# Performance work log

Measured on AMD Instinct MI355X. Metric: run time of the kernel, lower is better.

Reference implementation:

```python
import jax, jax.numpy as jnp
import numpy as np

SCALE = 1.0 / np.sqrt(128.0)  # 1/sqrt(head_size)
NEG = -1000000000.0


def setup_inputs() -> dict:
    key = jax.random.key(0)
    k1, k2, k3, k4 = jax.random.split(key, 4)
    B, H, S, D = 2, 16, 2048, 128
    q = jax.random.normal(k1, (B, H, S, D), dtype=jnp.float32)
    k = jax.random.normal(k2, (B, H, S, D), dtype=jnp.float32)
    v = jax.random.normal(k3, (B, H, S, D), dtype=jnp.float32)
    mask = jax.random.randint(k4, (B, S), 0, 2, dtype=jnp.int32)
    return {"q": q, "k": k, "v": v, "mask": mask}


def reference(q, k, v, mask):
    # scores: [B, H, Sq, Sk]
    scores = jnp.einsum("bhqd,bhkd->bhqk", q, k) * SCALE
    m = mask[:, None, None, :]  # [B,1,1,Sk], broadcast over heads and queries
    scores = jnp.where(m == 0, NEG, scores)
    weights = jax.nn.softmax(scores, axis=-1)
    out = jnp.einsum("bhqk,bhkd->bhqd", weights, v)
    return out
```

## Files before the change

### kernel.cpp

```cpp
#include <hip/hip_runtime.h>
#include <hip/hip_bf16.h>

typedef __attribute__((ext_vector_type(8))) short short8;
typedef __attribute__((ext_vector_type(4))) short short4v;
typedef __attribute__((ext_vector_type(4))) float floatx4;

#define NB 2
#define NH 16
#define NBH 32
#define SS 2048
#define DD 128
#define BQ 128
#define BK 32
#define KTILES (SS / BK)
#define SCALE 0.08838834764831845f
#define LOG2E 1.4426950408889634f
#define MAXB 12.0f
#define MASKED_BIAS -100000.0f

#define WC_VM4 0x0F74
#define WC_VM0 0x0F70
#define WC_LGKM0 0xC07F

__device__ __forceinline__ short f2bf(float f) {
  union { float f; unsigned u; } x; x.f = f;
  return (short)((x.u + 0x7FFFu + ((x.u >> 16) & 1u)) >> 16);
}

__device__ __forceinline__ void pack8(short8* dst, float a, float b, float c, float d,
                                      float e, float f, float g, float h) {
  union { __hip_bfloat162 h2[4]; short8 v; } u;
  u.h2[0] = __float22bfloat162_rn(make_float2(a, b));
  u.h2[1] = __float22bfloat162_rn(make_float2(c, d));
  u.h2[2] = __float22bfloat162_rn(make_float2(e, f));
  u.h2[3] = __float22bfloat162_rn(make_float2(g, h));
  *dst = u.v;
}

__device__ __forceinline__ void gload_lds16(const short* g, short* l) {
  __builtin_amdgcn_global_load_lds(
      (const __attribute__((address_space(1))) void*)(g),
      (__attribute__((address_space(3))) void*)(l), 16, 0, 0);
}

__global__ __launch_bounds__(256) void prep_kernel(const float* __restrict__ k,
                                                   const float* __restrict__ v,
                                                   short* __restrict__ kbf,
                                                   short* __restrict__ vtg) {
  __shared__ short Ts[DD][68];
  const int kb = blockIdx.x, bh = blockIdx.y;
  const int tid = threadIdx.x;
  const size_t base = (size_t)bh * SS * DD + (size_t)(kb * 64) * DD;
  const float* kr = k + base;
  const float* vr = v + base;
  short* kw = kbf + base;
#pragma unroll
  for (int c = 0; c < 8; ++c) {
    int fi = c * 256 + tid;
    float4 a = ((const float4*)kr)[fi];
    short4v o;
    o[0] = f2bf(a.x); o[1] = f2bf(a.y); o[2] = f2bf(a.z); o[3] = f2bf(a.w);
    *(short4v*)(kw + (size_t)fi * 4) = o;
    float4 vv = ((const float4*)vr)[fi];
    int d0 = (fi * 4) & 127, key = (fi * 4) >> 7;
    Ts[d0 + 0][key] = f2bf(vv.x);
    Ts[d0 + 1][key] = f2bf(vv.y);
    Ts[d0 + 2][key] = f2bf(vv.z);
    Ts[d0 + 3][key] = f2bf(vv.w);
  }
  __syncthreads();
#pragma unroll
  for (int s = 0; s < 4; ++s) {
    int d = s * 32 + (tid >> 3);
    int c = tid & 7, kt2 = c >> 2, g = c & 3;
    short4v lo = *(short4v*)&Ts[d][kt2 * 32 + g * 4];
    short4v hi = *(short4v*)&Ts[d][kt2 * 32 + 16 + g * 4];
    short8 o;
#pragma unroll
    for (int r = 0; r < 4; ++r) { o[r] = lo[r]; o[4 + r] = hi[r]; }
    *(short8*)(vtg + ((size_t)(bh * DD + d)) * SS + (kb * 2 + kt2) * 32 + g * 8) = o;
  }
}

__global__ __launch_bounds__(256, 2) void fa_kernel(
    const float* __restrict__ q, const short* __restrict__ kbf,
    const short* __restrict__ vtg, const int* __restrict__ mask,
    float* __restrict__ out) {
  __shared__ __align__(16) short Ks[3][BK * DD];
  __shared__ __align__(16) short Vt[3][DD * BK];
  __shared__ float Bias[SS];

  const int tid = threadIdx.x;
  const int wave = tid >> 6;
  const int lane = tid & 63;
  const int l16 = lane & 15;
  const int quad = lane >> 4;
  const int bh = blockIdx.y;
  const int b = bh >> 4;
  const int q0 = blockIdx.x * BQ;

  const size_t base = (size_t)bh * SS * DD;
  const float* qg = q + base;
  const short* kg = kbf + base;
  const short* vgb = vtg + (size_t)bh * DD * SS;
  const int* mg = mask + b * SS;
  const float c1 = SCALE * LOG2E, c2 = MAXB * LOG2E;

  short8 qf[2][4];
#pragma unroll
  for (int t = 0; t < 2; ++t) {
    const float* qp = qg + (size_t)(q0 + wave * 32 + t * 16 + l16) * DD;
#pragma unroll
    for (int dc = 0; dc < 4; ++dc) {
      float4 a = *(const float4*)(qp + dc * 32 + quad * 8);
      float4 bb = *(const float4*)(qp + dc * 32 + quad * 8 + 4);
      short8 tt;
      tt[0] = f2bf(a.x); tt[1] = f2bf(a.y); tt[2] = f2bf(a.z); tt[3] = f2bf(a.w);
      tt[4] = f2bf(bb.x); tt[5] = f2bf(bb.y); tt[6] = f2bf(bb.z); tt[7] = f2bf(bb.w);
      qf[t][dc] = tt;
    }
  }

  {
    int i0 = tid * 8;
    int4 m0 = *(const int4*)(mg + i0);
    int4 m1 = *(const int4*)(mg + i0 + 4);
    float4 f0, f1;
    f0.x = m0.x ? -c2 : MASKED_BIAS; f0.y = m0.y ? -c2 : MASKED_BIAS;
    f0.z = m0.z ? -c2 : MASKED_BIAS; f0.w = m0.w ? -c2 : MASKED_BIAS;
    f1.x = m1.x ? -c2 : MASKED_BIAS; f1.y = m1.y ? -c2 : MASKED_BIAS;
    f1.z = m1.z ? -c2 : MASKED_BIAS; f1.w = m1.w ? -c2 : MASKED_BIAS;
    *(float4*)&Bias[i0] = f0;
    *(float4*)&Bias[i0 + 4] = f1;
  }

  floatx4 Oacc[2][8];
#pragma unroll
  for (int t = 0; t < 2; ++t)
#pragma unroll
    for (int f = 0; f < 8; ++f) Oacc[t][f] = (floatx4){0.f, 0.f, 0.f, 0.f};
  float l_acc[2] = {0.f, 0.f};

  const short* kpg[2];
  const short* vpg[2];
  int kls[2], vls[2];
#pragma unroll
  for (int i = 0; i < 2; ++i) {
    int c = wave * 2 + i;
    int krow = c * 4 + (lane >> 4);
    kpg[i] = kg + (size_t)krow * DD + (((lane & 15) ^ (krow & 7)) * 8);
    int d = c * 16 + (lane >> 2);
    vpg[i] = vgb + (size_t)d * SS + (((lane & 3) ^ ((lane >> 3) & 3)) * 8);
    kls[i] = c * 512;
    vls[i] = c * 512;
  }

  int koff[2];
#pragma unroll
  for (int nt = 0; nt < 2; ++nt) koff[nt] = (nt * 16 + l16) * DD;
  const int ksw = l16 & 7;
  const int voff = l16 * 32 + ((quad ^ ((l16 >> 1) & 3)) * 8);

#pragma unroll
  for (int i = 0; i < 2; ++i) {
    gload_lds16(kpg[i], &Ks[0][kls[i]]);
    gload_lds16(vpg[i], &Vt[0][vls[i]]);
  }
#pragma unroll
  for (int i = 0; i < 2; ++i) {
    gload_lds16(kpg[i] + (size_t)BK * DD, &Ks[1][kls[i]]);
    gload_lds16(vpg[i] + BK, &Vt[1][vls[i]]);
  }
  __builtin_amdgcn_s_waitcnt(WC_LGKM0);

  int cur = 0;
#pragma unroll 1
  for (int kt = 0; kt < KTILES; ++kt) {
    if (kt + 1 < KTILES) __builtin_amdgcn_s_waitcnt(WC_VM4);
    else                 __builtin_amdgcn_s_waitcnt(WC_VM0);
    __builtin_amdgcn_s_barrier();

    int ibuf = cur + 2; if (ibuf >= 3) ibuf -= 3;
    if (kt + 2 < KTILES) {
      const size_t kadv = (size_t)(kt + 2) * (BK * DD);
      const int vadv = (kt + 2) * BK;
#pragma unroll
      for (int i = 0; i < 2; ++i) {
        gload_lds16(kpg[i] + kadv, &Ks[ibuf][kls[i]]);
        gload_lds16(vpg[i] + vadv, &Vt[ibuf][vls[i]]);
      }
    }

    float4 bb0 = *(const float4*)&Bias[kt * 32 + quad * 4];
    float4 bb1 = *(const float4*)&Bias[kt * 32 + 16 + quad * 4];

    const short* ksb = &Ks[cur][0];
    const short* vsb = &Vt[cur][0];
    floatx4 sacc[2][2];
#pragma unroll
    for (int t = 0; t < 2; ++t)
#pragma unroll
      for (int nt = 0; nt < 2; ++nt) sacc[t][nt] = (floatx4){0.f, 0.f, 0.f, 0.f};
#pragma unroll
    for (int nt = 0; nt < 2; ++nt)
#pragma unroll
      for (int dc = 0; dc < 4; ++dc) {
        short8 kf = *(const short8*)(ksb + koff[nt] + (((dc * 4 + quad) ^ ksw) * 8));
        sacc[0][nt] = __builtin_amdgcn_mfma_f32_16x16x32_bf16(kf, qf[0][dc], sacc[0][nt], 0, 0, 0);
        sacc[1][nt] = __builtin_amdgcn_mfma_f32_16x16x32_bf16(kf, qf[1][dc], sacc[1][nt], 0, 0, 0);
      }

    short8 pb[2];
#pragma unroll
    for (int t = 0; t < 2; ++t) {
      float e0 = __builtin_amdgcn_exp2f(fmaf(sacc[t][0][0], c1, bb0.x));
      float e1 = __builtin_amdgcn_exp2f(fmaf(sacc[t][0][1], c1, bb0.y));
      float e2 = __builtin_amdgcn_exp2f(fmaf(sacc[t][0][2], c1, bb0.z));
      float e3 = __builtin_amdgcn_exp2f(fmaf(sacc[t][0][3], c1, bb0.w));
      float g0 = __builtin_amdgcn_exp2f(fmaf(sacc[t][1][0], c1, bb1.x));
      float g1 = __builtin_amdgcn_exp2f(fmaf(sacc[t][1][1], c1, bb1.y));
      float g2 = __builtin_amdgcn_exp2f(fmaf(sacc[t][1][2], c1, bb1.z));
      float g3 = __builtin_amdgcn_exp2f(fmaf(sacc[t][1][3], c1, bb1.w));
      l_acc[t] += ((e0 + e1) + (e2 + e3)) + ((g0 + g1) + (g2 + g3));
      pack8(&pb[t], e0, e1, e2, e3, g0, g1, g2, g3);
    }

#pragma unroll
    for (int f = 0; f < 8; ++f) {
      short8 vv = *(const short8*)(vsb + f * 512 + voff);
      Oacc[0][f] = __builtin_amdgcn_mfma_f32_16x16x32_bf16(vv, pb[0], Oacc[0][f], 0, 0, 0);
      Oacc[1][f] = __builtin_amdgcn_mfma_f32_16x16x32_bf16(vv, pb[1], Oacc[1][f], 0, 0, 0);
    }

    cur = cur + 1; if (cur >= 3) cur = 0;
  }

  float* og = out + base;
#pragma unroll
  for (int t = 0; t < 2; ++t) {
    float s = l_acc[t];
    s += __shfl_xor(s, 16);
    s += __shfl_xor(s, 32);
    float inv = 1.0f / s;
    float* orow = og + (size_t)(q0 + wave * 32 + t * 16 + l16) * DD + quad * 4;
#pragma unroll
    for (int f = 0; f < 8; ++f) {
      float4 w;
      w.x = Oacc[t][f][0] * inv;
      w.y = Oacc[t][f][1] * inv;
      w.z = Oacc[t][f][2] * inv;
      w.w = Oacc[t][f][3] * inv;
      *(float4*)(orow + f * 16) = w;
    }
  }
}

extern "C" void kernel_launch(void* const* d_in, const int* in_sizes, int n_in,
                              void* d_out, int out_size, void* d_ws, size_t ws_size,
                              hipStream_t stream) {
  const float* q = (const float*)d_in[0];
  const float* k = (const float*)d_in[1];
  const float* v = (const float*)d_in[2];
  const int* mask = (const int*)d_in[3];
  float* out = (float*)d_out;

  short* kbf = (short*)d_ws;
  short* vtg = kbf + (size_t)NBH * SS * DD;

  prep_kernel<<<dim3(SS / 64, NBH), dim3(256), 0, stream>>>(k, v, kbf, vtg);
  fa_kernel<<<dim3(SS / BQ, NBH), dim3(256), 0, stream>>>(q, kbf, vtg, mask, out);
}
```

Baseline: 210.7 us.

## Swizzle prep transpose, remap blocks, stagger K start, move prefetch after QK, set priorities

The prep kernel's V transpose now loads 4x4 float4 blocks and writes XOR-swizzled short4 vectors into LDS, replacing scalar padded stores, to cut LDS bank conflicts. The attention kernel remaps block IDs so neighbouring blocks spread across heads, and some heads start the K-tile loop at an offset, aiming to reduce L2/HBM hotspotting on the same K/V tiles. The next-tile prefetch is issued after the QK MFMAs instead of before, and s_setprio raises wave priority around the MFMA sections to interleave math with other waves' softmax. These changes bundle several unrelated ideas and could shift scheduling in either direction.

```diff
diff --git a/kernel.cpp b/kernel.cpp
--- a/kernel.cpp
+++ b/kernel.cpp
@@ -47,13 +47,14 @@
                                                    const float* __restrict__ v,
                                                    short* __restrict__ kbf,
                                                    short* __restrict__ vtg) {
-  __shared__ short Ts[DD][68];
+  __shared__ __align__(16) short Ts[DD * 64];
   const int kb = blockIdx.x, bh = blockIdx.y;
   const int tid = threadIdx.x;
   const size_t base = (size_t)bh * SS * DD + (size_t)(kb * 64) * DD;
   const float* kr = k + base;
   const float* vr = v + base;
   short* kw = kbf + base;
+
 #pragma unroll
   for (int c = 0; c < 8; ++c) {
     int fi = c * 256 + tid;
@@ -61,20 +62,38 @@
     short4v o;
     o[0] = f2bf(a.x); o[1] = f2bf(a.y); o[2] = f2bf(a.z); o[3] = f2bf(a.w);
     *(short4v*)(kw + (size_t)fi * 4) = o;
-    float4 vv = ((const float4*)vr)[fi];
-    int d0 = (fi * 4) & 127, key = (fi * 4) >> 7;
-    Ts[d0 + 0][key] = f2bf(vv.x);
-    Ts[d0 + 1][key] = f2bf(vv.y);
-    Ts[d0 + 2][key] = f2bf(vv.z);
-    Ts[d0 + 3][key] = f2bf(vv.w);
+  }
+
+  const int kg = tid & 15;
+  const int dg0 = tid >> 4;
+#pragma unroll
+  for (int c = 0; c < 2; ++c) {
+    int dg = dg0 + 16 * c;
+    float rr[4][4];
+#pragma unroll
+    for (int r = 0; r < 4; ++r) {
+      float4 a = ((const float4*)vr)[(kg * 4 + r) * 32 + dg];
+      rr[r][0] = a.x; rr[r][1] = a.y; rr[r][2] = a.z; rr[r][3] = a.w;
+    }
+#pragma unroll
+    for (int j = 0; j < 4; ++j) {
+      int d = dg * 4 + j;
+      short4v t;
+      t[0] = f2bf(rr[0][j]); t[1] = f2bf(rr[1][j]);
+      t[2] = f2bf(rr[2][j]); t[3] = f2bf(rr[3][j]);
+      int si = d * 64 + (((kg * 8) ^ ((d & 15) << 3)) >> 1);
+      *(short4v*)&Ts[si] = t;
+    }
   }
   __syncthreads();
+
 #pragma unroll
   for (int s = 0; s < 4; ++s) {
     int d = s * 32 + (tid >> 3);
     int c = tid & 7, kt2 = c >> 2, g = c & 3;
-    short4v lo = *(short4v*)&Ts[d][kt2 * 32 + g * 4];
-    short4v hi = *(short4v*)&Ts[d][kt2 * 32 + 16 + g * 4];
+    int x = (d & 15) << 3;
+    short4v lo = *(short4v*)&Ts[d * 64 + ((((kt2 * 8 + g) * 8) ^ x) >> 1)];
+    short4v hi = *(short4v*)&Ts[d * 64 + ((((kt2 * 8 + g + 4) * 8) ^ x) >> 1)];
     short8 o;
 #pragma unroll
     for (int r = 0; r < 4; ++r) { o[r] = lo[r]; o[4 + r] = hi[r]; }
@@ -95,9 +114,13 @@
   const int lane = tid & 63;
   const int l16 = lane & 15;
   const int quad = lane >> 4;
-  const int bh = blockIdx.y;
+
+  const int lid = blockIdx.y * 16 + blockIdx.x;
+  const int vid = (lid & 7) * 64 + (lid >> 3);
+  const int bh = vid >> 4;
+  const int q0 = (vid & 15) * BQ;
   const int b = bh >> 4;
-  const int q0 = blockIdx.x * BQ;
+  const int kt0off = ((bh >> 1) & 1) << 5;
 
   const size_t base = (size_t)bh * SS * DD;
   const float* qg = q + base;
@@ -161,35 +184,29 @@
   const int ksw = l16 & 7;
   const int voff = l16 * 32 + ((quad ^ ((l16 >> 1) & 3)) * 8);
 
-#pragma unroll
-  for (int i = 0; i < 2; ++i) {
-    gload_lds16(kpg[i], &Ks[0][kls[i]]);
-    gload_lds16(vpg[i], &Vt[0][vls[i]]);
-  }
-#pragma unroll
-  for (int i = 0; i < 2; ++i) {
-    gload_lds16(kpg[i] + (size_t)BK * DD, &Ks[1][kls[i]]);
-    gload_lds16(vpg[i] + BK, &Vt[1][vls[i]]);
+  {
+    const size_t ka0 = (size_t)kt0off * (BK * DD);
+    const int va0 = kt0off * BK;
+#pragma unroll
+    for (int i = 0; i < 2; ++i) {
+      gload_lds16(kpg[i] + ka0, &Ks[0][kls[i]]);
+      gload_lds16(vpg[i] + va0, &Vt[0][vls[i]]);
+    }
+#pragma unroll
+    for (int i = 0; i < 2; ++i) {
+      gload_lds16(kpg[i] + ka0 + (size_t)(BK * DD), &Ks[1][kls[i]]);
+      gload_lds16(vpg[i] + va0 + BK, &Vt[1][vls[i]]);
+    }
   }
   __builtin_amdgcn_s_waitcnt(WC_LGKM0);
 
   int cur = 0;
 #pragma unroll 1
-  for (int kt = 0; kt < KTILES; ++kt) {
-    if (kt + 1 < KTILES) __builtin_amdgcn_s_waitcnt(WC_VM4);
+  for (int it = 0; it < KTILES; ++it) {
+    const int kt = (it + kt0off) & (KTILES - 1);
+    if (it + 1 < KTILES) __builtin_amdgcn_s_waitcnt(WC_VM4);
     else                 __builtin_amdgcn_s_waitcnt(WC_VM0);
     __builtin_amdgcn_s_barrier();
-
-    int ibuf = cur + 2; if (ibuf >= 3) ibuf -= 3;
-    if (kt + 2 < KTILES) {
-      const size_t kadv = (size_t)(kt + 2) * (BK * DD);
-      const int vadv = (kt + 2) * BK;
-#pragma unroll
-      for (int i = 0; i < 2; ++i) {
-        gload_lds16(kpg[i] + kadv, &Ks[ibuf][kls[i]]);
-        gload_lds16(vpg[i] + vadv, &Vt[ibuf][vls[i]]);
-      }
-    }
 
     float4 bb0 = *(const float4*)&Bias[kt * 32 + quad * 4];
     float4 bb1 = *(const float4*)&Bias[kt * 32 + 16 + quad * 4];
@@ -201,6 +218,7 @@
     for (int t = 0; t < 2; ++t)
 #pragma unroll
       for (int nt = 0; nt < 2; ++nt) sacc[t][nt] = (floatx4){0.f, 0.f, 0.f, 0.f};
+    __builtin_amdgcn_s_setprio(1);
 #pragma unroll
     for (int nt = 0; nt < 2; ++nt)
 #pragma unroll
@@ -209,6 +227,19 @@
         sacc[0][nt] = __builtin_amdgcn_mfma_f32_16x16x32_bf16(kf, qf[0][dc], sacc[0][nt], 0, 0, 0);
         sacc[1][nt] = __builtin_amdgcn_mfma_f32_16x16x32_bf16(kf, qf[1][dc], sacc[1][nt], 0, 0, 0);
       }
+    __builtin_amdgcn_s_setprio(0);
+
+    int ibuf = cur + 2; if (ibuf >= 3) ibuf -= 3;
+    if (it + 2 < KTILES) {
+      const int ktn = (it + 2 + kt0off) & (KTILES - 1);
+      const size_t kadv = (size_t)ktn * (BK * DD);
+      const int vadv = ktn * BK;
+#pragma unroll
+      for (int i = 0; i < 2; ++i) {
+        gload_lds16(kpg[i] + kadv, &Ks[ibuf][kls[i]]);
+        gload_lds16(vpg[i] + vadv, &Vt[ibuf][vls[i]]);
+      }
+    }
 
     short8 pb[2];
 #pragma unroll
@@ -225,12 +256,14 @@
       pack8(&pb[t], e0, e1, e2, e3, g0, g1, g2, g3);
     }
 
+    __builtin_amdgcn_s_setprio(1);
 #pragma unroll
     for (int f = 0; f < 8; ++f) {
       short8 vv = *(const short8*)(vsb + f * 512 + voff);
       Oacc[0][f] = __builtin_amdgcn_mfma_f32_16x16x32_bf16(vv, pb[0], Oacc[0][f], 0, 0, 0);
       Oacc[1][f] = __builtin_amdgcn_mfma_f32_16x16x32_bf16(vv, pb[1], Oacc[1][f], 0, 0, 0);
     }
+    __builtin_amdgcn_s_setprio(0);
 
     cur = cur + 1; if (cur >= 3) cur = 0;
   }
```

New measurement: 204.2 us. 1.03x faster.
